# Performance work log

Measured on AMD Instinct MI355X. Metric: run time of the kernel, lower is better.

The kernel has to match this reference:

```python
import jax, jax.numpy as jnp
import numpy as np

EPS = 1e-5

def fwht(x):
    """Normalized fast Walsh-Hadamard transform along the last axis (len must be power of 2)."""
    orig_shape = x.shape
    n = orig_shape[-1]
    x = x.reshape(-1, n)
    h = 1
    while h < n:
        x = x.reshape(-1, n // (2 * h), 2, h)
        a, b = x[:, :, 0, :], x[:, :, 1, :]
        x = jnp.stack([a + b, a - b], axis=2).reshape(-1, n)
        h *= 2
    return (x * (1.0 / np.sqrt(n))).reshape(orig_shape)

def act_quant(x):
    """Per-token 8-bit absmax activation quantization (BitNet), with STE identity."""
    scale = 127.0 / jnp.clip(jnp.max(jnp.abs(x), axis=-1, keepdims=True), EPS)
    q = jnp.clip(jnp.round(x * scale), -128.0, 127.0) / scale
    return x + jax.lax.stop_gradient(q - x)

def weight_quant(w):
    """Ternary (1.58-bit) absmean weight quantization (BitNet b1.58), with STE identity."""
    scale = jnp.clip(jnp.mean(jnp.abs(w)), EPS)
    q = jnp.clip(jnp.round(w / scale), -1.0, 1.0) * scale
    return w + jax.lax.stop_gradient(q - w)

def h_bitlinear(x, w):
    """EnhancedHBitLinear: Hadamard-rotate activations, quantize acts+weights, matmul."""
    xq = act_quant(fwht(x))
    wq = weight_quant(w)
    return jnp.einsum('bsh,oh->bso', xq, wq)

def setup_inputs() -> dict:
    key = jax.random.key(0)
    k1, k2, k3, k4 = jax.random.split(key, 4)
    H, I = 2048, 8192
    B, S = 2, 2048
    hidden_states = jax.random.normal(k1, (B, S, H), dtype=jnp.float32)
    w_gate = jax.random.normal(k2, (I, H), dtype=jnp.float32) * 0.02
    w_up = jax.random.normal(k3, (I, H), dtype=jnp.float32) * 0.02
    w_down = jax.random.normal(k4, (H, I), dtype=jnp.float32) * 0.02
    return {"hidden_states": hidden_states, "w_gate": w_gate, "w_up": w_up, "w_down": w_down}

def reference(hidden_states, w_gate, w_up, w_down):
    gate = h_bitlinear(hidden_states, w_gate)          # [B,S,I]
    up = h_bitlinear(hidden_states, w_up)              # [B,S,I]
    return h_bitlinear(jax.nn.silu(gate) * up, w_down)  # [B,S,H]
```

## Files before the change

### kernel.cpp

```cpp
#include <hip/hip_runtime.h>
#include <math.h>

#define EPSF 1e-5f

typedef __attribute__((ext_vector_type(4))) int i32x4;

__device__ __forceinline__ void gload_lds16(const void* g, void* l) {
  __builtin_amdgcn_global_load_lds(
      (const __attribute__((address_space(1))) void*)g,
      (__attribute__((address_space(3))) void*)l, 16, 0, 0);
}

__global__ void zero_sums_kernel(double* sums) {
  if (threadIdx.x < 3) sums[threadIdx.x] = 0.0;
}

__global__ __launch_bounds__(256) void absmean_kernel(
    const float* __restrict__ wg, const float* __restrict__ wu,
    const float* __restrict__ wd, double* __restrict__ sums) {
  const int N4 = 16777216 / 4;
  const float* W = (blockIdx.y == 0) ? wg : ((blockIdx.y == 1) ? wu : wd);
  double acc = 0.0;
  const int stride = gridDim.x * 256;
  for (int i = blockIdx.x * 256 + threadIdx.x; i < N4; i += stride) {
    float4 v = ((const float4*)W)[i];
    acc += (double)fabsf(v.x);
    acc += (double)fabsf(v.y);
    acc += (double)fabsf(v.z);
    acc += (double)fabsf(v.w);
  }
  for (int o = 32; o > 0; o >>= 1) acc += __shfl_down(acc, o);
  __shared__ double sred[4];
  const int wid = threadIdx.x >> 6, lane = threadIdx.x & 63;
  if (lane == 0) sred[wid] = acc;
  __syncthreads();
  if (threadIdx.x == 0)
    atomicAdd(&sums[blockIdx.y], sred[0] + sred[1] + sred[2] + sred[3]);
}

__global__ __launch_bounds__(256) void wquant_kernel(
    const float* __restrict__ wg, const float* __restrict__ wu,
    const float* __restrict__ wd, signed char* __restrict__ qg,
    signed char* __restrict__ qu, signed char* __restrict__ qd,
    const double* __restrict__ sums, float* __restrict__ scalef) {
  const int mat = blockIdx.y;
  const float* W = (mat == 0) ? wg : ((mat == 1) ? wu : wd);
  signed char* Q = (mat == 0) ? qg : ((mat == 1) ? qu : qd);
  const float scale = fmaxf((float)(sums[mat] * (1.0 / 16777216.0)), EPSF);
  if (blockIdx.x == 0 && threadIdx.x == 0) scalef[mat] = scale;
  const int i = blockIdx.x * 256 + threadIdx.x;
  float4 v = ((const float4*)W)[i];
  int q0 = (int)fminf(fmaxf(rintf(v.x / scale), -1.f), 1.f);
  int q1 = (int)fminf(fmaxf(rintf(v.y / scale), -1.f), 1.f);
  int q2 = (int)fminf(fmaxf(rintf(v.z / scale), -1.f), 1.f);
  int q3 = (int)fminf(fmaxf(rintf(v.w / scale), -1.f), 1.f);
  int packed = (q0 & 0xff) | ((q1 & 0xff) << 8) | ((q2 & 0xff) << 16) | (q3 << 24);
  ((int*)Q)[i] = packed;
}

template <int N>
__global__ __launch_bounds__(256) void fwht_quant_kernel(
    const float* __restrict__ X, signed char* __restrict__ Q,
    float* __restrict__ drow, float cnorm) {
  __shared__ float s[N];
  __shared__ float red[4];
  const int tid = threadIdx.x;
  const size_t row = blockIdx.x;
  const float* x = X + row * (size_t)N;
  for (int i = tid; i < N / 4; i += 256)
    ((float4*)s)[i] = ((const float4*)x)[i];
  __syncthreads();
  for (int h = 1; h < N; h <<= 1) {
    for (int p = tid; p < N / 2; p += 256) {
      int i = ((p & ~(h - 1)) << 1) | (p & (h - 1));
      int j = i + h;
      float a = s[i], b = s[j];
      s[i] = a + b;
      s[j] = a - b;
    }
    __syncthreads();
  }
  const int PER = N / 256;
  float m = 0.f;
  for (int i = tid * PER; i < tid * PER + PER; ++i) m = fmaxf(m, fabsf(s[i]));
  for (int o = 32; o > 0; o >>= 1) m = fmaxf(m, __shfl_xor(m, o));
  const int wid = tid >> 6, lane = tid & 63;
  if (lane == 0) red[wid] = m;
  __syncthreads();
  m = fmaxf(fmaxf(red[0], red[1]), fmaxf(red[2], red[3]));
  const float maxv = fmaxf(m * cnorm, EPSF);
  const float scale = 127.0f / maxv;
  if (tid == 0) drow[row] = maxv / 127.0f;
  const size_t qbase = row * (size_t)N + (size_t)tid * PER;
#pragma unroll
  for (int i0 = 0; i0 < PER; i0 += 4) {
    int q[4];
#pragma unroll
    for (int k = 0; k < 4; ++k) {
      float y = s[tid * PER + i0 + k] * cnorm;
      float qf = rintf(y * scale);
      qf = fminf(fmaxf(qf, -128.f), 127.f);
      q[k] = (int)qf;
    }
    int packed =
        (q[0] & 0xff) | ((q[1] & 0xff) << 8) | ((q[2] & 0xff) << 16) | (q[3] << 24);
    *(int*)(Q + qbase + i0) = packed;
  }
}

__global__ __launch_bounds__(256) void gemm1_kernel(
    const signed char* __restrict__ Aq, const signed char* __restrict__ Bg,
    const signed char* __restrict__ Bu, const float* __restrict__ drow,
    const float* __restrict__ scalef, float* __restrict__ H) {
  const int K = 2048;
  __shared__ __align__(16) signed char sA[2][128 * 64];
  __shared__ __align__(16) signed char sG[2][128 * 64];
  __shared__ __align__(16) signed char sU[2][128 * 64];
  const int tid = threadIdx.x;
  const int wid = tid >> 6;
  const int lane = tid & 63;
  const int wr = wid >> 1, wc = wid & 1;
  const int mbase = blockIdx.y * 128, nbase = blockIdx.x * 128;
  const int srow = tid >> 2;
  const int scol = (tid & 3) << 4;

  const signed char* gA = Aq + (size_t)(mbase + srow) * K + scol;
  const signed char* gG = Bg + (size_t)(nbase + srow) * K + scol;
  const signed char* gU = Bu + (size_t)(nbase + srow) * K + scol;

  i32x4 accG[4][4] = {};
  i32x4 accU[4][4] = {};

  auto stage = [&](int buf, int kk) {
    const size_t o = (size_t)kk;
    const int lb = wid << 10;
    gload_lds16(gA + o, &sA[buf][lb]);
    gload_lds16(gA + o + (size_t)64 * K, &sA[buf][4096 + lb]);
    gload_lds16(gG + o, &sG[buf][lb]);
    gload_lds16(gG + o + (size_t)64 * K, &sG[buf][4096 + lb]);
    gload_lds16(gU + o, &sU[buf][lb]);
    gload_lds16(gU + o + (size_t)64 * K, &sU[buf][4096 + lb]);
  };

  stage(0, 0);
  __syncthreads();
  int cur = 0;
  const int ko = (lane >> 4) << 4;
  const int rA = (wr << 6) + (lane & 15);
  const int rB = (wc << 6) + (lane & 15);
  for (int t = 0; t < K / 64; ++t) {
    if (t + 1 < K / 64) stage(cur ^ 1, (t + 1) * 64);
    i32x4 a[4], bg[4], bu[4];
#pragma unroll
    for (int m = 0; m < 4; ++m)
      a[m] = *(const i32x4*)&sA[cur][(rA + m * 16) * 64 + ko];
#pragma unroll
    for (int n = 0; n < 4; ++n) {
      bg[n] = *(const i32x4*)&sG[cur][(rB + n * 16) * 64 + ko];
      bu[n] = *(const i32x4*)&sU[cur][(rB + n * 16) * 64 + ko];
    }
#pragma unroll
    for (int m = 0; m < 4; ++m)
#pragma unroll
      for (int n = 0; n < 4; ++n) {
        accG[m][n] =
            __builtin_amdgcn_mfma_i32_16x16x64_i8(a[m], bg[n], accG[m][n], 0, 0, 0);
        accU[m][n] =
            __builtin_amdgcn_mfma_i32_16x16x64_i8(a[m], bu[n], accU[m][n], 0, 0, 0);
      }
    __syncthreads();
    cur ^= 1;
  }

  const float sg = scalef[0], su = scalef[1];
  const int orow = (lane >> 4) << 2;
  const int ocol = lane & 15;
#pragma unroll
  for (int m = 0; m < 4; ++m)
#pragma unroll
    for (int n = 0; n < 4; ++n)
#pragma unroll
      for (int j = 0; j < 4; ++j) {
        int grow = mbase + (wr << 6) + m * 16 + orow + j;
        int gcol = nbase + (wc << 6) + n * 16 + ocol;
        float dr = drow[grow];
        float gate = (float)accG[m][n][j] * (sg * dr);
        float up = (float)accU[m][n][j] * (su * dr);
        float hval = (gate / (1.0f + expf(-gate))) * up;
        H[(size_t)grow * 8192 + gcol] = hval;
      }
}

__global__ __launch_bounds__(256) void gemm2_kernel(
    const signed char* __restrict__ Aq, const signed char* __restrict__ Bq,
    const float* __restrict__ drow, const float* __restrict__ scalef,
    float* __restrict__ O) {
  const int K = 8192;
  __shared__ __align__(16) signed char sA[2][128 * 64];
  __shared__ __align__(16) signed char sB[2][128 * 64];
  const int tid = threadIdx.x;
  const int wid = tid >> 6;
  const int lane = tid & 63;
  const int wr = wid >> 1, wc = wid & 1;
  const int mbase = blockIdx.y * 128, nbase = blockIdx.x * 128;
  const int srow = tid >> 2;
  const int scol = (tid & 3) << 4;

  const signed char* gA = Aq + (size_t)(mbase + srow) * K + scol;
  const signed char* gB = Bq + (size_t)(nbase + srow) * K + scol;

  i32x4 acc[4][4] = {};

  auto stage = [&](int buf, int kk) {
    const size_t o = (size_t)kk;
    const int lb = wid << 10;
    gload_lds16(gA + o, &sA[buf][lb]);
    gload_lds16(gA + o + (size_t)64 * K, &sA[buf][4096 + lb]);
    gload_lds16(gB + o, &sB[buf][lb]);
    gload_lds16(gB + o + (size_t)64 * K, &sB[buf][4096 + lb]);
  };

  stage(0, 0);
  __syncthreads();
  int cur = 0;
  const int ko = (lane >> 4) << 4;
  const int rA = (wr << 6) + (lane & 15);
  const int rB = (wc << 6) + (lane & 15);
  for (int t = 0; t < K / 64; ++t) {
    if (t + 1 < K / 64) stage(cur ^ 1, (t + 1) * 64);
    i32x4 a[4], b[4];
#pragma unroll
    for (int m = 0; m < 4; ++m)
      a[m] = *(const i32x4*)&sA[cur][(rA + m * 16) * 64 + ko];
#pragma unroll
    for (int n = 0; n < 4; ++n)
      b[n] = *(const i32x4*)&sB[cur][(rB + n * 16) * 64 + ko];
#pragma unroll
    for (int m = 0; m < 4; ++m)
#pragma unroll
      for (int n = 0; n < 4; ++n)
        acc[m][n] = __builtin_amdgcn_mfma_i32_16x16x64_i8(a[m], b[n], acc[m][n], 0, 0, 0);
    __syncthreads();
    cur ^= 1;
  }

  const float sd = scalef[2];
  const int orow = (lane >> 4) << 2;
  const int ocol = lane & 15;
#pragma unroll
  for (int m = 0; m < 4; ++m)
#pragma unroll
    for (int n = 0; n < 4; ++n)
#pragma unroll
      for (int j = 0; j < 4; ++j) {
        int grow = mbase + (wr << 6) + m * 16 + orow + j;
        int gcol = nbase + (wc << 6) + n * 16 + ocol;
        O[(size_t)grow * 2048 + gcol] = (float)acc[m][n][j] * (sd * drow[grow]);
      }
}

extern "C" void kernel_launch(void* const* d_in, const int* in_sizes, int n_in,
                              void* d_out, int out_size, void* d_ws, size_t ws_size,
                              hipStream_t stream) {
  (void)in_sizes; (void)n_in; (void)out_size; (void)ws_size;
  const float* x = (const float*)d_in[0];
  const float* wg = (const float*)d_in[1];
  const float* wu = (const float*)d_in[2];
  const float* wd = (const float*)d_in[3];
  float* out = (float*)d_out;

  char* ws = (char*)d_ws;
  double* sums = (double*)ws;
  float* scalef = (float*)(ws + 256);
  size_t off = 1024;
  signed char* qg = (signed char*)(ws + off); off += 16777216;
  signed char* qu = (signed char*)(ws + off); off += 16777216;
  signed char* qd = (signed char*)(ws + off); off += 16777216;
  signed char* xq = (signed char*)(ws + off); off += 8388608;
  signed char* hq = (signed char*)(ws + off); off += 33554432;
  float* dr1 = (float*)(ws + off); off += 16384;
  float* dr2 = (float*)(ws + off); off += 16384;
  float* Hbuf = (float*)(ws + off); off += (size_t)4096 * 8192 * 4;

  zero_sums_kernel<<<1, 64, 0, stream>>>(sums);
  absmean_kernel<<<dim3(1024, 3), 256, 0, stream>>>(wg, wu, wd, sums);
  wquant_kernel<<<dim3(16384, 3), 256, 0, stream>>>(wg, wu, wd, qg, qu, qd, sums,
                                                    scalef);
  const float c1 = (float)(1.0 / sqrt(2048.0));
  const float c2 = (float)(1.0 / sqrt(8192.0));
  fwht_quant_kernel<2048><<<4096, 256, 0, stream>>>(x, xq, dr1, c1);
  gemm1_kernel<<<dim3(64, 32), 256, 0, stream>>>(xq, qg, qu, dr1, scalef, Hbuf);
  fwht_quant_kernel<8192><<<4096, 256, 0, stream>>>(Hbuf, hq, dr2, c2);
  gemm2_kernel<<<dim3(16, 32), 256, 0, stream>>>(hq, qd, dr2, scalef, out);
}
```

Baseline: 712.2 us.

## Triple-buffer int8 GEMM pipelines with XOR LDS swizzle and block-order swizzle

Both int8 MFMA GEMMs move from double to triple buffering, with explicit vmcnt waits and raw s_barrier so two tiles of global-to-LDS loads stay in flight. LDS columns are XOR-swizzled to reduce bank conflicts on the 16-byte fragment reads. Block indices are remapped so neighbouring workgroups share A/B tiles in L2, and s_setprio raises wave priority around the MFMA section. The larger LDS footprint and launch-bound occupancy hints may limit resident blocks, and the hand-written waitcnt logic is fragile.

Measured after the change: 630.6 us. 11.4% less time.

```diff
diff --git a/kernel.cpp b/kernel.cpp
--- a/kernel.cpp
+++ b/kernel.cpp
@@ -4,6 +4,9 @@
 #define EPSF 1e-5f
 
 typedef __attribute__((ext_vector_type(4))) int i32x4;
+
+#define S_WAITCNT_VMCNT(N) asm volatile("s_waitcnt vmcnt(" #N ")" ::: "memory")
+#define S_WAITCNT_LGKM0() asm volatile("s_waitcnt lgkmcnt(0)" ::: "memory")
 
 __device__ __forceinline__ void gload_lds16(const void* g, void* l) {
   __builtin_amdgcn_global_load_lds(
@@ -108,22 +111,24 @@
   }
 }
 
-__global__ __launch_bounds__(256) void gemm1_kernel(
+__global__ __launch_bounds__(256, 2) void gemm1_kernel(
     const signed char* __restrict__ Aq, const signed char* __restrict__ Bg,
     const signed char* __restrict__ Bu, const float* __restrict__ drow,
     const float* __restrict__ scalef, float* __restrict__ H) {
-  const int K = 2048;
-  __shared__ __align__(16) signed char sA[2][128 * 64];
-  __shared__ __align__(16) signed char sG[2][128 * 64];
-  __shared__ __align__(16) signed char sU[2][128 * 64];
+  const int K = 2048, T = K / 64;
+  const int BUF = 24576;
+  __shared__ __align__(16) signed char smem[3 * BUF];
   const int tid = threadIdx.x;
   const int wid = tid >> 6;
   const int lane = tid & 63;
   const int wr = wid >> 1, wc = wid & 1;
-  const int mbase = blockIdx.y * 128, nbase = blockIdx.x * 128;
+
+  const int orig = blockIdx.y * 64 + blockIdx.x;
+  const int swz = (orig & 7) * 256 + (orig >> 3);
+  const int mbase = (swz >> 6) * 128, nbase = (swz & 63) * 128;
+
   const int srow = tid >> 2;
-  const int scol = (tid & 3) << 4;
-
+  const int scol = (((tid & 3) ^ ((srow >> 1) & 3)) << 4);
   const signed char* gA = Aq + (size_t)(mbase + srow) * K + scol;
   const signed char* gG = Bg + (size_t)(nbase + srow) * K + scol;
   const signed char* gU = Bu + (size_t)(nbase + srow) * K + scol;
@@ -131,34 +136,40 @@
   i32x4 accG[4][4] = {};
   i32x4 accU[4][4] = {};
 
-  auto stage = [&](int buf, int kk) {
+  auto stage = [&](int boff, int kk) {
     const size_t o = (size_t)kk;
-    const int lb = wid << 10;
-    gload_lds16(gA + o, &sA[buf][lb]);
-    gload_lds16(gA + o + (size_t)64 * K, &sA[buf][4096 + lb]);
-    gload_lds16(gG + o, &sG[buf][lb]);
-    gload_lds16(gG + o + (size_t)64 * K, &sG[buf][4096 + lb]);
-    gload_lds16(gU + o, &sU[buf][lb]);
-    gload_lds16(gU + o + (size_t)64 * K, &sU[buf][4096 + lb]);
+    const int lb = boff + (wid << 10);
+    gload_lds16(gA + o, &smem[lb]);
+    gload_lds16(gA + o + (size_t)64 * K, &smem[lb + 4096]);
+    gload_lds16(gG + o, &smem[lb + 8192]);
+    gload_lds16(gG + o + (size_t)64 * K, &smem[lb + 12288]);
+    gload_lds16(gU + o, &smem[lb + 16384]);
+    gload_lds16(gU + o + (size_t)64 * K, &smem[lb + 20480]);
   };
 
-  stage(0, 0);
-  __syncthreads();
-  int cur = 0;
-  const int ko = (lane >> 4) << 4;
+  const int kos = (((lane >> 4) ^ ((lane >> 1) & 3)) << 4);
   const int rA = (wr << 6) + (lane & 15);
   const int rB = (wc << 6) + (lane & 15);
-  for (int t = 0; t < K / 64; ++t) {
-    if (t + 1 < K / 64) stage(cur ^ 1, (t + 1) * 64);
+
+  stage(0, 0);
+  stage(BUF, 64);
+  int bc = 0, bn = BUF, bf = 2 * BUF;
+  for (int t = 0; t < T; ++t) {
+    S_WAITCNT_VMCNT(6);
+    __builtin_amdgcn_s_barrier();
+    __builtin_amdgcn_sched_barrier(0);
+    const int kk = (t + 2 < T) ? (t + 2) * 64 : (T - 1) * 64;
+    stage(bf, kk);
     i32x4 a[4], bg[4], bu[4];
 #pragma unroll
     for (int m = 0; m < 4; ++m)
-      a[m] = *(const i32x4*)&sA[cur][(rA + m * 16) * 64 + ko];
+      a[m] = *(const i32x4*)&smem[bc + (rA + m * 16) * 64 + kos];
 #pragma unroll
     for (int n = 0; n < 4; ++n) {
-      bg[n] = *(const i32x4*)&sG[cur][(rB + n * 16) * 64 + ko];
-      bu[n] = *(const i32x4*)&sU[cur][(rB + n * 16) * 64 + ko];
+      bg[n] = *(const i32x4*)&smem[bc + 8192 + (rB + n * 16) * 64 + kos];
+      bu[n] = *(const i32x4*)&smem[bc + 16384 + (rB + n * 16) * 64 + kos];
     }
+    __builtin_amdgcn_s_setprio(1);
 #pragma unroll
     for (int m = 0; m < 4; ++m)
 #pragma unroll
@@ -168,8 +179,10 @@
         accU[m][n] =
             __builtin_amdgcn_mfma_i32_16x16x64_i8(a[m], bu[n], accU[m][n], 0, 0, 0);
       }
-    __syncthreads();
-    cur ^= 1;
+    __builtin_amdgcn_s_setprio(0);
+    S_WAITCNT_LGKM0();
+    __builtin_amdgcn_sched_barrier(0);
+    const int tmp = bc; bc = bn; bn = bf; bf = tmp;
   }
 
   const float sg = scalef[0], su = scalef[1];
@@ -191,57 +204,68 @@
       }
 }
 
-__global__ __launch_bounds__(256) void gemm2_kernel(
+__global__ __launch_bounds__(256, 3) void gemm2_kernel(
     const signed char* __restrict__ Aq, const signed char* __restrict__ Bq,
     const float* __restrict__ drow, const float* __restrict__ scalef,
     float* __restrict__ O) {
-  const int K = 8192;
-  __shared__ __align__(16) signed char sA[2][128 * 64];
-  __shared__ __align__(16) signed char sB[2][128 * 64];
+  const int K = 8192, T = K / 64;
+  const int BUF = 16384;
+  __shared__ __align__(16) signed char smem[3 * BUF];
   const int tid = threadIdx.x;
   const int wid = tid >> 6;
   const int lane = tid & 63;
   const int wr = wid >> 1, wc = wid & 1;
-  const int mbase = blockIdx.y * 128, nbase = blockIdx.x * 128;
+
+  const int orig = blockIdx.y * 16 + blockIdx.x;
+  const int swz = (orig & 7) * 64 + (orig >> 3);
+  const int mbase = (swz >> 4) * 128, nbase = (swz & 15) * 128;
+
   const int srow = tid >> 2;
-  const int scol = (tid & 3) << 4;
-
+  const int scol = (((tid & 3) ^ ((srow >> 1) & 3)) << 4);
   const signed char* gA = Aq + (size_t)(mbase + srow) * K + scol;
   const signed char* gB = Bq + (size_t)(nbase + srow) * K + scol;
 
   i32x4 acc[4][4] = {};
 
-  auto stage = [&](int buf, int kk) {
+  auto stage = [&](int boff, int kk) {
     const size_t o = (size_t)kk;
-    const int lb = wid << 10;
-    gload_lds16(gA + o, &sA[buf][lb]);
-    gload_lds16(gA + o + (size_t)64 * K, &sA[buf][4096 + lb]);
-    gload_lds16(gB + o, &sB[buf][lb]);
-    gload_lds16(gB + o + (size_t)64 * K, &sB[buf][4096 + lb]);
+    const int lb = boff + (wid << 10);
+    gload_lds16(gA + o, &smem[lb]);
+    gload_lds16(gA + o + (size_t)64 * K, &smem[lb + 4096]);
+    gload_lds16(gB + o, &smem[lb + 8192]);
+    gload_lds16(gB + o + (size_t)64 * K, &smem[lb + 12288]);
   };
 
-  stage(0, 0);
-  __syncthreads();
-  int cur = 0;
-  const int ko = (lane >> 4) << 4;
+  const int kos = (((lane >> 4) ^ ((lane >> 1) & 3)) << 4);
   const int rA = (wr << 6) + (lane & 15);
   const int rB = (wc << 6) + (lane & 15);
-  for (int t = 0; t < K / 64; ++t) {
-    if (t + 1 < K / 64) stage(cur ^ 1, (t + 1) * 64);
+
+  stage(0, 0);
+  stage(BUF, 64);
+  int bc = 0, bn = BUF, bf = 2 * BUF;
+  for (int t = 0; t < T; ++t) {
+    S_WAITCNT_VMCNT(4);
+    __builtin_amdgcn_s_barrier();
+    __builtin_amdgcn_sched_barrier(0);
+    const int kk = (t + 2 < T) ? (t + 2) * 64 : (T - 1) * 64;
+    stage(bf, kk);
     i32x4 a[4], b[4];
 #pragma unroll
     for (int m = 0; m < 4; ++m)
-      a[m] = *(const i32x4*)&sA[cur][(rA + m * 16) * 64 + ko];
+      a[m] = *(const i32x4*)&smem[bc + (rA + m * 16) * 64 + kos];
 #pragma unroll
     for (int n = 0; n < 4; ++n)
-      b[n] = *(const i32x4*)&sB[cur][(rB + n * 16) * 64 + ko];
+      b[n] = *(const i32x4*)&smem[bc + 8192 + (rB + n * 16) * 64 + kos];
+    __builtin_amdgcn_s_setprio(1);
 #pragma unroll
     for (int m = 0; m < 4; ++m)
 #pragma unroll
       for (int n = 0; n < 4; ++n)
         acc[m][n] = __builtin_amdgcn_mfma_i32_16x16x64_i8(a[m], b[n], acc[m][n], 0, 0, 0);
-    __syncthreads();
-    cur ^= 1;
+    __builtin_amdgcn_s_setprio(0);
+    S_WAITCNT_LGKM0();
+    __builtin_amdgcn_sched_barrier(0);
+    const int tmp = bc; bc = bn; bn = bf; bf = tmp;
   }
 
   const float sd = scalef[2];
```
